# Kernel tuning notes

Measured on AMD Instinct MI355X. Metric: run time of the kernel, lower is better.

## Reference

```python
import jax, jax.numpy as jnp
import numpy as np
from jax import lax

WINDOW_SIZE = 11
SIGMA = 1.5
MAX_VAL = 1.0
C1 = (0.01 * MAX_VAL) ** 2
C2 = (0.03 * MAX_VAL) ** 2
PAD = (WINDOW_SIZE - 1) // 2


def _gaussian_kernel2d(ksize: int, sigma: float) -> jnp.ndarray:
    x = jnp.arange(ksize, dtype=jnp.float32) - ksize // 2
    g = jnp.exp(-(x ** 2) / (2.0 * sigma ** 2))
    g = g / jnp.sum(g)
    return jnp.outer(g, g)  # [k, k]


def _filter2d(x: jnp.ndarray, kernel2d: jnp.ndarray) -> jnp.ndarray:
    # depthwise conv: x [B,C,H,W], kernel repeated per channel -> [C,1,k,k]
    c = x.shape[1]
    k = jnp.broadcast_to(kernel2d[None, None], (c, 1, WINDOW_SIZE, WINDOW_SIZE)).astype(x.dtype)
    return lax.conv_general_dilated(
        x, k,
        window_strides=(1, 1),
        padding=((PAD, PAD), (PAD, PAD)),
        dimension_numbers=("NCHW", "OIHW", "NCHW"),
        feature_group_count=c,
    )


def setup_inputs() -> dict:
    key = jax.random.key(0)
    k1, k2 = jax.random.split(key)
    img1 = jax.random.uniform(k1, (16, 3, 512, 512), dtype=jnp.float32)
    img2 = jax.random.uniform(k2, (16, 3, 512, 512), dtype=jnp.float32)
    return {"img1": img1, "img2": img2}


def reference(img1, img2):
    kernel = _gaussian_kernel2d(WINDOW_SIZE, SIGMA)
    mu1 = _filter2d(img1, kernel)
    mu2 = _filter2d(img2, kernel)
    mu1_sq = mu1 * mu1
    mu2_sq = mu2 * mu2
    mu1_mu2 = mu1 * mu2
    sigma1_sq = _filter2d(img1 * img1, kernel) - mu1_sq
    sigma2_sq = _filter2d(img2 * img2, kernel) - mu2_sq
    sigma12 = _filter2d(img1 * img2, kernel) - mu1_mu2
    ssim_map = ((2.0 * mu1_mu2 + C1) * (2.0 * sigma12 + C2)) / (
        (mu1_sq + mu2_sq + C1) * (sigma1_sq + sigma2_sq + C2)
    )
    loss = jnp.clip(1.0 - ssim_map, 0.0, 1.0) / 2.0
    return jnp.mean(loss)  # reduction='mean'
```

## Files before the change

kernel.cpp:

```cpp
#include <hip/hip_runtime.h>


#define BATCH  16
#define CHAN   3
#define H_     512
#define W_     512
#define HW     (H_ * W_)
#define CH_H   64
#define NPIX   ((long)BATCH*CHAN*H_*W_)

#define GW0 0.0010284f
#define GW1 0.0075988f
#define GW2 0.0360008f
#define GW3 0.1093554f
#define GW4 0.2130056f
#define GW5 0.2660117f

typedef float v2 __attribute__((ext_vector_type(2)));

__device__ __forceinline__ float wg(int k) {
    return (k == 0 || k == 10) ? GW0
         : (k == 1 || k == 9)  ? GW1
         : (k == 2 || k == 8)  ? GW2
         : (k == 3 || k == 7)  ? GW3
         : (k == 4 || k == 6)  ? GW4 : GW5;
}

__device__ __forceinline__ v2 pfma(v2 a, v2 b, v2 c) {
#if __has_builtin(__builtin_elementwise_fma)
    return __builtin_elementwise_fma(a, b, c);
#else
    v2 r; r.x = fmaf(a.x, b.x, c.x); r.y = fmaf(a.y, b.y, c.y); return r;
#endif
}
__device__ __forceinline__ v2 psfma(float s, v2 b, v2 c) {
    v2 sv; sv.x = s; sv.y = s;
    return pfma(sv, b, c);
}

__device__ __forceinline__ float ssim_retire(float mu1, float mu2,
                                             float x11, float x22, float x12) {
    const float c1 = 1.0e-4f;
    const float c2 = 9.0e-4f;
    float mu1s = mu1 * mu1;
    float mu2s = mu2 * mu2;
    float m12  = mu1 * mu2;
    float num  = (2.0f * m12 + c1) * (2.0f * (x12 - m12) + c2);
    float den  = (mu1s + mu2s + c1) * ((x11 - mu1s) + (x22 - mu2s) + c2);
    float l = 1.0f - num / den;
    return fminf(fmaxf(l, 0.0f), 1.0f);
}

#define DECL(i) v2 P##i = {0.f, 0.f}, Q##i = {0.f, 0.f}; float E##i = 0.f
#define ACCI(i) do { const float wj_ = wg(10 - (i));             \
    P##i = psfma(wj_, hmm, P##i);                                \
    Q##i = psfma(wj_, hss, Q##i);                                \
    E##i = fmaf(wj_, hm12, E##i); } while (0)
#define SHIFT(i, j) P##i = P##j; Q##i = Q##j; E##i = E##j

__global__ __launch_bounds__(256, 3) void ssim_kernel(const float* __restrict__ img1,
                                                      const float* __restrict__ img2,
                                                      float* __restrict__ out) {
    __shared__ __align__(16) v2 sp[4][80];
    __shared__ float wsum[4];

    const int tid  = threadIdx.x;
    const int lane = tid & 63;
    const int wv   = tid >> 6;

    const int wid   = blockIdx.x * 4 + wv;
    const int plane = wid >> 6;
    const int rem   = wid & 63;
    const int strip = rem & 7;
    const int chunk = rem >> 3;
    const int y0 = chunk * CH_H;
    const int c0 = strip * 64;

    const int  colg  = c0 - 5 + lane;
    const bool colOk = (colg >= 0);
    const int  colC  = colOk ? colg : 0;
    const int  colg2  = c0 + 59 + lane;
    const bool colOk2 = (lane < 11) && (colg2 < W_);
    const int  col2C  = colOk2 ? colg2 : 0;

    const size_t pb = (size_t)plane * HW;
    const float* __restrict__ p1  = img1 + pb + colC;
    const float* __restrict__ p2  = img2 + pb + colC;
    const float* __restrict__ p1b = img1 + pb + col2C;
    const float* __restrict__ p2b = img2 + pb + col2C;

    v2* st = sp[wv];

    DECL(0); DECL(1); DECL(2); DECL(3); DECL(4); DECL(5);
    DECL(6); DECL(7); DECL(8); DECL(9); DECL(10);
    float lsum = 0.0f;

    float cv1, cv2, cv1b, cv2b;
    {
        int r = y0 - 5;
        bool rok = (unsigned)r < (unsigned)H_;
        size_t off = (size_t)(rok ? r : 0) * W_;
        cv1  = (rok && colOk)  ? p1[off]  : 0.0f;
        cv2  = (rok && colOk)  ? p2[off]  : 0.0f;
        cv1b = (rok && colOk2) ? p1b[off] : 0.0f;
        cv2b = (rok && colOk2) ? p2b[off] : 0.0f;
    }

#pragma unroll 2
    for (int step = 0; step < 74; ++step) {
        const int yy = step - 10;

        {
            v2 v; v.x = cv1; v.y = cv2;
            st[lane] = v;
            if (lane < 11) { v2 vb; vb.x = cv1b; vb.y = cv2b; st[64 + lane] = vb; }
        }
        __asm__ __volatile__("" ::: "memory");

        {
            int r = y0 + yy + 6;
            bool rok = (unsigned)r < (unsigned)H_;
            size_t off = (size_t)(rok ? r : 0) * W_;
            cv1  = (rok && colOk)  ? p1[off]  : 0.0f;
            cv2  = (rok && colOk)  ? p2[off]  : 0.0f;
            cv1b = (rok && colOk2) ? p1b[off] : 0.0f;
            cv2b = (rok && colOk2) ? p2b[off] : 0.0f;
        }

        v2 hmm = {0.f, 0.f}, hss = {0.f, 0.f};
        float hm12 = 0.f;
#pragma unroll
        for (int k = 0; k < 11; ++k) {
            v2 ab = st[lane + k];
            float wk = wg(k);
            v2 t = ab;
            t.x *= wk; t.y *= wk;
            hmm += t;
            hss = pfma(t, ab, hss);
            hm12 = fmaf(t.x, ab.y, hm12);
        }
        __asm__ __volatile__("" ::: "memory");

        ACCI(0); ACCI(1); ACCI(2); ACCI(3); ACCI(4); ACCI(5);
        ACCI(6); ACCI(7); ACCI(8); ACCI(9); ACCI(10);

        if (yy >= 0) lsum += ssim_retire(P0.x, P0.y, Q0.x, Q0.y, E0);

        SHIFT(0, 1); SHIFT(1, 2); SHIFT(2, 3); SHIFT(3, 4); SHIFT(4, 5);
        SHIFT(5, 6); SHIFT(6, 7); SHIFT(7, 8); SHIFT(8, 9); SHIFT(9, 10);
        P10 = (v2){0.f, 0.f}; Q10 = (v2){0.f, 0.f}; E10 = 0.f;
    }

#pragma unroll
    for (int off = 32; off > 0; off >>= 1) lsum += __shfl_down(lsum, off);
    if (lane == 0) wsum[wv] = lsum;
    __syncthreads();
    if (tid == 0) {
        float bs = wsum[0] + wsum[1] + wsum[2] + wsum[3];
        atomicAdd(out, bs * (0.5f / (float)NPIX));
    }
}

extern "C" void kernel_launch(void* const* d_in, const int* in_sizes, int n_in,
                              void* d_out, int out_size, void* d_ws, size_t ws_size,
                              hipStream_t stream) {
    const float* img1 = (const float*)d_in[0];
    const float* img2 = (const float*)d_in[1];
    float* out = (float*)d_out;

    hipMemsetAsync(out, 0, sizeof(float), stream);

    ssim_kernel<<<dim3(8 * 8 * BATCH * CHAN / 4), 256, 0, stream>>>(img1, img2, out);
}
```

Baseline: 155.0 us.

## Halve row chunks, rotate accumulator registers by unrolling, raise occupancy

Row chunks per wave shrink from 64 to 32, which doubles the number of waves and blocks. The 11 vertical accumulators now rotate by name across an 11-step unrolled loop instead of being shifted each step, so the per-step register moves go away. Launch bounds are raised to 5 blocks per SM and the division is replaced by a hardware reciprocal. Each chunk now rereads a 10-row halo relative to only 32 output rows instead of 64, so redundant loads and compute grow. The reciprocal is also slightly less accurate.

```diff
diff --git a/kernel.cpp b/kernel.cpp
--- a/kernel.cpp
+++ b/kernel.cpp
@@ -6,7 +6,7 @@
 #define H_     512
 #define W_     512
 #define HW     (H_ * W_)
-#define CH_H   64
+#define CH_H   32
 #define NPIX   ((long)BATCH*CHAN*H_*W_)
 
 #define GW0 0.0010284f
@@ -47,18 +47,75 @@
     float m12  = mu1 * mu2;
     float num  = (2.0f * m12 + c1) * (2.0f * (x12 - m12) + c2);
     float den  = (mu1s + mu2s + c1) * ((x11 - mu1s) + (x22 - mu2s) + c2);
-    float l = 1.0f - num / den;
+    float l = 1.0f - num * __builtin_amdgcn_rcpf(den);
     return fminf(fmaxf(l, 0.0f), 1.0f);
 }
 
 #define DECL(i) v2 P##i = {0.f, 0.f}, Q##i = {0.f, 0.f}; float E##i = 0.f
-#define ACCI(i) do { const float wj_ = wg(10 - (i));             \
-    P##i = psfma(wj_, hmm, P##i);                                \
-    Q##i = psfma(wj_, hss, Q##i);                                \
-    E##i = fmaf(wj_, hm12, E##i); } while (0)
-#define SHIFT(i, j) P##i = P##j; Q##i = Q##j; E##i = E##j
 
-__global__ __launch_bounds__(256, 3) void ssim_kernel(const float* __restrict__ img1,
+#define ACCW(s, wi)                          \
+    P##s = psfma(wg(wi), hmm, P##s);         \
+    Q##s = psfma(wg(wi), hss, Q##s);         \
+    E##s = fmaf(wg(wi), hm12, E##s);
+
+#define ACCSET(s)                            \
+    P##s.x = GW0 * hmm.x; P##s.y = GW0 * hmm.y;  \
+    Q##s.x = GW0 * hss.x; Q##s.y = GW0 * hss.y;  \
+    E##s = GW0 * hm12;
+
+#define PH_ACC(s0,s1,s2,s3,s4,s5,s6,s7,s8,s9,s10)                       \
+    ACCW(s0,10) ACCW(s1,9) ACCW(s2,8) ACCW(s3,7) ACCW(s4,6) ACCW(s5,5)  \
+    ACCW(s6,4)  ACCW(s7,3) ACCW(s8,2) ACCW(s9,1) ACCSET(s10)
+
+#define STEP(s0,s1,s2,s3,s4,s5,s6,s7,s8,s9,s10) do {                    \
+    st[lane] = cur;                                                     \
+    if (lane < 11) st[64 + lane] = curb;                                \
+    __asm__ __volatile__("" ::: "memory");                              \
+    rr += 1;                                                            \
+    {                                                                   \
+        bool rok = (unsigned)rr < (unsigned)H_;                         \
+        size_t off = (size_t)(rok ? rr : 0) * W_;                       \
+        float x1 = p1[off], x2 = p2[off];                               \
+        float xb1 = 0.f, xb2 = 0.f;                                     \
+        if (lane < 11) { xb1 = p1b[off]; xb2 = p2b[off]; }              \
+        nxt.x  = (rok && colOk)  ? x1  : 0.f;                           \
+        nxt.y  = (rok && colOk)  ? x2  : 0.f;                           \
+        nxtb.x = (rok && colOk2) ? xb1 : 0.f;                           \
+        nxtb.y = (rok && colOk2) ? xb2 : 0.f;                           \
+    }                                                                   \
+    v2 hmm = {0.f, 0.f}, hss = {0.f, 0.f};                              \
+    float hm12 = 0.f;                                                   \
+    _Pragma("unroll")                                                   \
+    for (int k = 0; k < 11; ++k) {                                      \
+        v2 ab = st[lane + k];                                           \
+        float wk = wg(k);                                               \
+        v2 t = ab; t.x *= wk; t.y *= wk;                                \
+        hmm += t;                                                       \
+        hss = pfma(t, ab, hss);                                         \
+        hm12 = fmaf(t.x, ab.y, hm12);                                   \
+    }                                                                   \
+    __asm__ __volatile__("" ::: "memory");                              \
+    PH_ACC(s0,s1,s2,s3,s4,s5,s6,s7,s8,s9,s10)                           \
+    if ((unsigned)yy < (unsigned)CH_H)                                  \
+        lsum += ssim_retire(P##s0.x, P##s0.y, Q##s0.x, Q##s0.y, E##s0); \
+    ++yy;                                                               \
+    cur = nxt; curb = nxtb;                                             \
+} while (0)
+
+#define RSTEP(R) STEP(R)
+#define ROT0  0,1,2,3,4,5,6,7,8,9,10
+#define ROT1  1,2,3,4,5,6,7,8,9,10,0
+#define ROT2  2,3,4,5,6,7,8,9,10,0,1
+#define ROT3  3,4,5,6,7,8,9,10,0,1,2
+#define ROT4  4,5,6,7,8,9,10,0,1,2,3
+#define ROT5  5,6,7,8,9,10,0,1,2,3,4
+#define ROT6  6,7,8,9,10,0,1,2,3,4,5
+#define ROT7  7,8,9,10,0,1,2,3,4,5,6
+#define ROT8  8,9,10,0,1,2,3,4,5,6,7
+#define ROT9  9,10,0,1,2,3,4,5,6,7,8
+#define ROT10 10,0,1,2,3,4,5,6,7,8,9
+
+__global__ __launch_bounds__(256, 5) void ssim_kernel(const float* __restrict__ img1,
                                                       const float* __restrict__ img2,
                                                       float* __restrict__ out) {
     __shared__ __align__(16) v2 sp[4][80];
@@ -69,8 +126,8 @@
     const int wv   = tid >> 6;
 
     const int wid   = blockIdx.x * 4 + wv;
-    const int plane = wid >> 6;
-    const int rem   = wid & 63;
+    const int plane = wid >> 7;
+    const int rem   = wid & 127;
     const int strip = rem & 7;
     const int chunk = rem >> 3;
     const int y0 = chunk * CH_H;
@@ -95,60 +152,25 @@
     DECL(6); DECL(7); DECL(8); DECL(9); DECL(10);
     float lsum = 0.0f;
 
-    float cv1, cv2, cv1b, cv2b;
+    int rr = y0 - 5;
+    int yy = -10;
+    v2 cur, curb, nxt = {0.f, 0.f}, nxtb = {0.f, 0.f};
     {
-        int r = y0 - 5;
-        bool rok = (unsigned)r < (unsigned)H_;
-        size_t off = (size_t)(rok ? r : 0) * W_;
-        cv1  = (rok && colOk)  ? p1[off]  : 0.0f;
-        cv2  = (rok && colOk)  ? p2[off]  : 0.0f;
-        cv1b = (rok && colOk2) ? p1b[off] : 0.0f;
-        cv2b = (rok && colOk2) ? p2b[off] : 0.0f;
+        bool rok = (unsigned)rr < (unsigned)H_;
+        size_t off = (size_t)(rok ? rr : 0) * W_;
+        float x1 = p1[off], x2 = p2[off];
+        float xb1 = 0.f, xb2 = 0.f;
+        if (lane < 11) { xb1 = p1b[off]; xb2 = p2b[off]; }
+        cur.x  = (rok && colOk)  ? x1  : 0.f;
+        cur.y  = (rok && colOk)  ? x2  : 0.f;
+        curb.x = (rok && colOk2) ? xb1 : 0.f;
+        curb.y = (rok && colOk2) ? xb2 : 0.f;
     }
 
-#pragma unroll 2
-    for (int step = 0; step < 74; ++step) {
-        const int yy = step - 10;
-
-        {
-            v2 v; v.x = cv1; v.y = cv2;
-            st[lane] = v;
-            if (lane < 11) { v2 vb; vb.x = cv1b; vb.y = cv2b; st[64 + lane] = vb; }
-        }
-        __asm__ __volatile__("" ::: "memory");
-
-        {
-            int r = y0 + yy + 6;
-            bool rok = (unsigned)r < (unsigned)H_;
-            size_t off = (size_t)(rok ? r : 0) * W_;
-            cv1  = (rok && colOk)  ? p1[off]  : 0.0f;
-            cv2  = (rok && colOk)  ? p2[off]  : 0.0f;
-            cv1b = (rok && colOk2) ? p1b[off] : 0.0f;
-            cv2b = (rok && colOk2) ? p2b[off] : 0.0f;
-        }
-
-        v2 hmm = {0.f, 0.f}, hss = {0.f, 0.f};
-        float hm12 = 0.f;
-#pragma unroll
-        for (int k = 0; k < 11; ++k) {
-            v2 ab = st[lane + k];
-            float wk = wg(k);
-            v2 t = ab;
-            t.x *= wk; t.y *= wk;
-            hmm += t;
-            hss = pfma(t, ab, hss);
-            hm12 = fmaf(t.x, ab.y, hm12);
-        }
-        __asm__ __volatile__("" ::: "memory");
-
-        ACCI(0); ACCI(1); ACCI(2); ACCI(3); ACCI(4); ACCI(5);
-        ACCI(6); ACCI(7); ACCI(8); ACCI(9); ACCI(10);
-
-        if (yy >= 0) lsum += ssim_retire(P0.x, P0.y, Q0.x, Q0.y, E0);
-
-        SHIFT(0, 1); SHIFT(1, 2); SHIFT(2, 3); SHIFT(3, 4); SHIFT(4, 5);
-        SHIFT(5, 6); SHIFT(6, 7); SHIFT(7, 8); SHIFT(8, 9); SHIFT(9, 10);
-        P10 = (v2){0.f, 0.f}; Q10 = (v2){0.f, 0.f}; E10 = 0.f;
+    for (int t = 0; t < 4; ++t) {
+        RSTEP(ROT0); RSTEP(ROT1); RSTEP(ROT2); RSTEP(ROT3); RSTEP(ROT4);
+        RSTEP(ROT5); RSTEP(ROT6); RSTEP(ROT7); RSTEP(ROT8); RSTEP(ROT9);
+        RSTEP(ROT10);
     }
 
 #pragma unroll
@@ -170,5 +192,5 @@
 
     hipMemsetAsync(out, 0, sizeof(float), stream);
 
-    ssim_kernel<<<dim3(8 * 8 * BATCH * CHAN / 4), 256, 0, stream>>>(img1, img2, out);
+    ssim_kernel<<<dim3(6144 / 4), 256, 0, stream>>>(img1, img2, out);
 }
```

Result: slower. 158.1 us (+2.1%).
